# Kernel optimization log

Hardware: AMD Instinct MI355X
Metric: run time of the kernel (lower is better)

Reference implementation:

```python
import jax, jax.numpy as jnp
import numpy as np

DIM = 2048
NUM_HEADS = 16
NUM_KV_HEADS = 4
HEAD_DIM = DIM // NUM_HEADS  # 128
KV_DIM = NUM_KV_HEADS * HEAD_DIM  # 512
ROPE_BASE = 10000.0
RMS_EPS = float(np.finfo(np.float32).eps)  # torch F.rms_norm default eps


def _rotary_tables(seq_len, dtype):
    inv_freq = 1.0 / (ROPE_BASE ** (jnp.arange(0, HEAD_DIM, 2, dtype=jnp.float32) / HEAD_DIM))
    freqs = jnp.arange(seq_len, dtype=jnp.float32)[:, None] * inv_freq[None, :]  # [S, hd/2]
    return jnp.cos(freqs).astype(dtype), jnp.sin(freqs).astype(dtype)


def _apply_rotary(x, cos, sin):
    # x: [B, H, S, hd]; cos/sin: [S, hd/2] broadcast over B,H
    half = x.shape[-1] // 2
    x1, x2 = x[..., :half], x[..., half:]
    return jnp.concatenate((x1 * cos + x2 * sin, x2 * cos - x1 * sin), axis=-1)


def _rms_norm(x):
    var = jnp.mean(jnp.square(x), axis=-1, keepdims=True)
    return x * jax.lax.rsqrt(var + RMS_EPS)


def setup_inputs() -> dict:
    key = jax.random.key(0)
    k1, k2, k3 = jax.random.split(key, 3)
    B, S = 4, 2048
    x = jax.random.normal(k1, (B, S, DIM), dtype=jnp.float32)
    W_qkv = jax.random.normal(k2, (DIM, DIM + 2 * KV_DIM), dtype=jnp.float32) * (DIM ** -0.5)
    W_out = jax.random.normal(k3, (DIM, DIM), dtype=jnp.float32) * (DIM ** -0.5)
    return {"x": x, "W_qkv": W_qkv, "W_out": W_out}


def reference(x, W_qkv, W_out):
    B, S, _ = x.shape
    G = NUM_HEADS // NUM_KV_HEADS  # GQA group size
    qkv = x @ W_qkv  # [B, S, dim + 2*kv_dim]
    q = qkv[..., :DIM].reshape(B, S, NUM_HEADS, HEAD_DIM).transpose(0, 2, 1, 3)
    k = qkv[..., DIM:DIM + KV_DIM].reshape(B, S, NUM_KV_HEADS, HEAD_DIM).transpose(0, 2, 1, 3)
    v = qkv[..., DIM + KV_DIM:].reshape(B, S, NUM_KV_HEADS, HEAD_DIM).transpose(0, 2, 1, 3)
    q = _rms_norm(q)
    k = _rms_norm(k)
    cos, sin = _rotary_tables(S, q.dtype)
    q = _apply_rotary(q, cos, sin)
    k = _apply_rotary(k, cos, sin)
    # Grouped-query attention without repeating K/V
    qg = q.reshape(B, NUM_KV_HEADS, G, S, HEAD_DIM)
    scale = HEAD_DIM ** -0.5
    scores = jnp.einsum('bkgsd,bktd->bkgst', qg, k) * scale  # [B, Hkv, G, S, S]
    causal = jnp.tril(jnp.ones((S, S), dtype=bool))
    scores = jnp.where(causal, scores, jnp.finfo(scores.dtype).min)
    probs = jax.nn.softmax(scores, axis=-1)
    y = jnp.einsum('bkgst,bktd->bkgsd', probs, v)  # [B, Hkv, G, S, hd]
    y = y.reshape(B, NUM_HEADS, S, HEAD_DIM).transpose(0, 2, 1, 3).reshape(B, S, DIM)
    return y @ W_out
```

## Files before the change

### kernel.cpp

```cpp
#include <hip/hip_runtime.h>

#define DIM    2048
#define SEQ    2048
#define BATCH  4
#define NH     16
#define NKV    4
#define HD     128
#define QKVN   3072
#define ROWS   (BATCH*SEQ)

typedef __bf16 bf16;
typedef __bf16 bf16x2 __attribute__((ext_vector_type(2)));
typedef __bf16 bf16x4 __attribute__((ext_vector_type(4)));
typedef __bf16 bf16x8 __attribute__((ext_vector_type(8)));
typedef float  f32x4  __attribute__((ext_vector_type(4)));
typedef float  f32x16 __attribute__((ext_vector_type(16)));

typedef union { bf16x4 v; unsigned int u[2]; } b4u;
typedef union { bf16x8 v8; bf16x4 v4[2]; } b8u;

#define SL2E 0.12752365234813963f

__device__ __forceinline__ void gload_lds16(const void* g, void* l) {
  __builtin_amdgcn_global_load_lds(
      (const __attribute__((address_space(1))) void*)g,
      (__attribute__((address_space(3))) void*)l, 16, 0, 0);
}


__global__ void convert_f32_bf16(const float* __restrict__ in, bf16* __restrict__ out, int n) {
  int i = (blockIdx.x * 256 + threadIdx.x) * 4;
  if (i < n) {
    float4 v = *(const float4*)(in + i);
    bf16x4 t = {(bf16)v.x, (bf16)v.y, (bf16)v.z, (bf16)v.w};
    *(bf16x4*)(out + i) = t;
  }
}

__global__ void transpose_w(const float* __restrict__ in, bf16* __restrict__ out, int R, int C) {
  __shared__ float t[64][65];
  int c0 = blockIdx.x * 64, r0 = blockIdx.y * 64;
  int tx = threadIdx.x & 63, ty = threadIdx.x >> 6;
  for (int i = ty; i < 64; i += 4) t[i][tx] = in[(size_t)(r0 + i) * C + c0 + tx];
  __syncthreads();
  for (int i = ty; i < 64; i += 4) out[(size_t)(c0 + i) * R + r0 + tx] = (bf16)t[tx][i];
}

__global__ void transpose_v(const bf16* __restrict__ vb, bf16* __restrict__ vT) {
  __shared__ bf16 t[64][65];
  int z = blockIdx.z;
  const bf16* in = vb + (size_t)z * SEQ * HD;
  bf16* out = vT + (size_t)z * HD * SEQ;
  int d0 = blockIdx.x * 64, s0 = blockIdx.y * 64;
  int tx = threadIdx.x & 63, ty = threadIdx.x >> 6;
  for (int i = ty; i < 64; i += 4) t[i][tx] = in[(size_t)(s0 + i) * HD + d0 + tx];
  __syncthreads();
  for (int i = ty; i < 64; i += 4) out[(size_t)(d0 + i) * SEQ + s0 + tx] = t[tx][i];
}

__global__ void rope_tables(float* __restrict__ cosT, float* __restrict__ sinT) {
  int idx = blockIdx.x * 256 + threadIdx.x;
  int s = idx >> 6, j = idx & 63;
  float inv = powf(10000.0f, -(float)j * (1.0f / 64.0f));
  float ang = (float)s * inv;
  cosT[idx] = cosf(ang);
  sinT[idx] = sinf(ang);
}

template <typename OutT>
__global__ __launch_bounds__(256, 2) void gemm_bt(
    const bf16* __restrict__ A, const bf16* __restrict__ BT,
    OutT* __restrict__ C, int M, int N, int K) {
  __shared__ __align__(16) bf16 lA[128 * 32];
  __shared__ __align__(16) bf16 lB[128 * 32];
  const int tid = threadIdx.x;
  const int lane = tid & 63, wave = tid >> 6;
  const int quad = lane >> 4, l16 = lane & 15;
  const int tileM = blockIdx.y * 128, tileN = blockIdx.x * 128;
  const int wm = (wave >> 1) * 64, wn = (wave & 1) * 64;

  f32x4 acc[4][4] = {};

  for (int kt = 0; kt < K; kt += 32) {
    __syncthreads();
    {
      int g0 = tid, g1 = tid + 256;
      gload_lds16(A + (size_t)(tileM + (g0 >> 2)) * K + kt + (g0 & 3) * 8,
                  (char*)lA + wave * 1024);
      gload_lds16(A + (size_t)(tileM + (g1 >> 2)) * K + kt + (g1 & 3) * 8,
                  (char*)lA + 4096 + wave * 1024);
      gload_lds16(BT + (size_t)(tileN + (g0 >> 2)) * K + kt + (g0 & 3) * 8,
                  (char*)lB + wave * 1024);
      gload_lds16(BT + (size_t)(tileN + (g1 >> 2)) * K + kt + (g1 & 3) * 8,
                  (char*)lB + 4096 + wave * 1024);
    }
    __syncthreads();

    bf16x8 af[4], bfr[4];
#pragma unroll
    for (int i = 0; i < 4; ++i)
      af[i] = *(const bf16x8*)&lA[(wm + i * 16 + l16) * 32 + quad * 8];
#pragma unroll
    for (int j = 0; j < 4; ++j)
      bfr[j] = *(const bf16x8*)&lB[(wn + j * 16 + l16) * 32 + quad * 8];
#pragma unroll
    for (int i = 0; i < 4; ++i)
#pragma unroll
      for (int j = 0; j < 4; ++j)
        acc[i][j] = __builtin_amdgcn_mfma_f32_16x16x32_bf16(af[i], bfr[j], acc[i][j], 0, 0, 0);
  }

#pragma unroll
  for (int i = 0; i < 4; ++i)
#pragma unroll
    for (int j = 0; j < 4; ++j)
#pragma unroll
      for (int r = 0; r < 4; ++r) {
        int row = tileM + wm + i * 16 + quad * 4 + r;
        int col = tileN + wn + j * 16 + l16;
        C[(size_t)row * N + col] = (OutT)acc[i][j][r];
      }
}

__global__ __launch_bounds__(256) void rmsnorm_rope(
    const bf16* __restrict__ qkv, const float* __restrict__ cosT,
    const float* __restrict__ sinT, bf16* __restrict__ qb,
    bf16* __restrict__ kb, bf16* __restrict__ vb) {
  int wave = threadIdx.x >> 6, lane = threadIdx.x & 63;
  int task = blockIdx.x * 4 + wave;
  int row = task / 24, chunk = task % 24;
  int b = row >> 11, s = row & 2047;

  const bf16* src = qkv + (size_t)row * QKVN + chunk * 128 + lane * 2;
  bf16x2 v = *(const bf16x2*)src;
  bf16 o0, o1;
  if (chunk >= 20) {
    o0 = v[0]; o1 = v[1];
  } else {
    float x0 = (float)v[0], x1 = (float)v[1];
    float ss = x0 * x0 + x1 * x1;
#pragma unroll
    for (int off = 1; off < 64; off <<= 1) ss += __shfl_xor(ss, off);
    float rms = rsqrtf(ss * (1.0f / 128.0f) + 1.1920929e-07f);
    x0 *= rms; x1 *= rms;
    float p0 = __shfl_xor(x0, 32), p1 = __shfl_xor(x1, 32);
    int j0 = (lane & 31) * 2;
    float c0 = cosT[s * 64 + j0], c1 = cosT[s * 64 + j0 + 1];
    float s0 = sinT[s * 64 + j0], s1 = sinT[s * 64 + j0 + 1];
    float r0, r1;
    if (lane < 32) { r0 = x0 * c0 + p0 * s0; r1 = x1 * c1 + p1 * s1; }
    else           { r0 = x0 * c0 - p0 * s0; r1 = x1 * c1 - p1 * s1; }
    if (chunk < 16) { r0 *= SL2E; r1 *= SL2E; }
    o0 = (bf16)r0; o1 = (bf16)r1;
  }
  bf16* dst;
  int d = lane * 2;
  if (chunk < 16)      dst = qb + ((size_t)(b * NH + chunk) * SEQ + s) * HD + d;
  else if (chunk < 20) dst = kb + ((size_t)(b * NKV + (chunk - 16)) * SEQ + s) * HD + d;
  else                 dst = vb + ((size_t)(b * NKV + (chunk - 20)) * SEQ + s) * HD + d;
  bf16x2 t = {o0, o1};
  *(bf16x2*)dst = t;
}

__global__ __launch_bounds__(256, 2) void attn_kernel(
    const bf16* __restrict__ qb, const bf16* __restrict__ kb,
    const bf16* __restrict__ vTb, bf16* __restrict__ y) {
  __shared__ __align__(16) char sm[65536];
  bf16* lK = (bf16*)sm;
  bf16* lV = (bf16*)(sm + 32768);

  const int tid = threadIdx.x;
  const int lane = tid & 63, wave = tid >> 6;
  const int l32 = lane & 31, h = lane >> 5;
  const int pairI = blockIdx.x, hh = blockIdx.y, b = blockIdx.z;
  const int kvh = hh >> 2;

  const bf16* qh = qb + (size_t)(b * NH + hh) * SEQ * HD;
  const bf16* kh = kb + (size_t)(b * NKV + kvh) * SEQ * HD;
  const bf16* vh = vTb + (size_t)(b * NKV + kvh) * HD * SEQ;

  for (int t = 0; t < 2; ++t) {
    const int qt = t ? pairI : (15 - pairI);
    const int qtile = qt * 128;
    const int qrow = qtile + wave * 32 + l32;

    bf16x8 qf[8];
#pragma unroll
    for (int ks = 0; ks < 8; ++ks)
      qf[ks] = *(const bf16x8*)&qh[(size_t)qrow * HD + ks * 16 + h * 8];

    f32x16 oacc[4] = {};
    float psum = 0.f;

    for (int kv0 = 0; kv0 <= qtile; kv0 += 128) {
      __syncthreads();
#pragma unroll
      for (int inst = 0; inst < 8; ++inst) {
        int slot = inst * 256 + tid;
        int R = slot >> 4;
        int gg = (slot & 15) ^ (R & 15);
        gload_lds16(kh + (size_t)(kv0 + R) * HD + gg * 8, (char*)lK + inst * 4096 + wave * 1024);
        gload_lds16(vh + (size_t)R * SEQ + kv0 + gg * 8, (char*)lV + inst * 4096 + wave * 1024);
      }
      __syncthreads();

      const bool diag = (kv0 == qtile);
      const int kvbMax = diag ? (wave + 1) : 4;
      for (int kvb = 0; kvb < kvbMax; ++kvb) {
        f32x16 sacc = {};
#pragma unroll
        for (int ks = 0; ks < 8; ++ks) {
          int row = kvb * 32 + l32;
          const bf16x8 af = *(const bf16x8*)&lK[row * 128 + (((ks * 2 + h) ^ (row & 15)) << 3)];
          sacc = __builtin_amdgcn_mfma_f32_32x32x16_bf16(af, qf[ks], sacc, 0, 0, 0);
        }
        float p[16];
        const bool msk = diag && (kvb == wave);
#pragma unroll
        for (int r = 0; r < 16; ++r) {
          float v = sacc[r];
          if (msk) {
            int kv = kv0 + kvb * 32 + (r & 3) + 4 * h + 8 * (r >> 2);
            if (kv > qrow) v = -1e30f;
          }
          float e = exp2f(v);
          p[r] = e;
          psum += e;
        }
        b4u pk[4];
#pragma unroll
        for (int B = 0; B < 4; ++B) {
          bf16x4 t4 = {(bf16)p[4 * B], (bf16)p[4 * B + 1], (bf16)p[4 * B + 2], (bf16)p[4 * B + 3]};
          pk[B].v = t4;
        }
#pragma unroll
        for (int ss = 0; ss < 2; ++ss) {
          b4u own = pk[2 * ss + h];
          b4u send = pk[2 * ss + (h ^ 1)];
          b4u got;
          got.u[0] = __shfl_xor(send.u[0], 32);
          got.u[1] = __shfl_xor(send.u[1], 32);
          b8u fr;
          fr.v4[0] = h ? got.v : own.v;
          fr.v4[1] = h ? own.v : got.v;
          int ks2 = kvb * 2 + ss;
#pragma unroll
          for (int nd = 0; nd < 4; ++nd) {
            int row = nd * 32 + l32;
            const bf16x8 vf = *(const bf16x8*)&lV[row * 128 + (((ks2 * 2 + h) ^ (row & 15)) << 3)];
            oacc[nd] = __builtin_amdgcn_mfma_f32_32x32x16_bf16(fr.v8, vf, oacc[nd], 0, 0, 0);
          }
        }
      }
    }

    float lsum = psum + __shfl_xor(psum, 32);
#pragma unroll
    for (int r = 0; r < 16; ++r) {
      int ql = (r & 3) + 4 * h + 8 * (r >> 2);
      float li = 1.0f / __shfl(lsum, ql);
      size_t base = ((size_t)(b * SEQ + qtile + wave * 32 + ql)) * DIM + hh * HD;
#pragma unroll
      for (int nd = 0; nd < 4; ++nd)
        y[base + nd * 32 + l32] = (bf16)(oacc[nd][r] * li);
    }
  }
}


extern "C" void kernel_launch(void* const* d_in, const int* in_sizes, int n_in,
                              void* d_out, int out_size, void* d_ws, size_t ws_size,
                              hipStream_t stream) {
  const float* x    = (const float*)d_in[0];
  const float* Wqkv = (const float*)d_in[1];
  const float* Wout = (const float*)d_in[2];
  float* out = (float*)d_out;

  char* w = (char*)d_ws;
  auto carve = [&](size_t bytes) -> char* {
    char* p = w;
    w += (bytes + 255) & ~(size_t)255;
    return p;
  };
  bf16* xb   = (bf16*)carve((size_t)ROWS * DIM * 2);
  bf16* WqT  = (bf16*)carve((size_t)QKVN * DIM * 2);
  bf16* WoT  = (bf16*)carve((size_t)DIM * DIM * 2);
  bf16* qkv  = (bf16*)carve((size_t)ROWS * QKVN * 2);
  bf16* kbuf = (bf16*)carve((size_t)BATCH * NKV * SEQ * HD * 2);
  bf16* vbuf = (bf16*)carve((size_t)BATCH * NKV * SEQ * HD * 2);
  float* cosT = (float*)carve((size_t)SEQ * 64 * 4);
  float* sinT = (float*)carve((size_t)SEQ * 64 * 4);

  bf16* qbuf = xb;
  bf16* vT   = WqT;
  bf16* ybuf = qkv;

  convert_f32_bf16<<<ROWS * DIM / 1024, 256, 0, stream>>>(x, xb, ROWS * DIM);
  transpose_w<<<dim3(QKVN / 64, DIM / 64), 256, 0, stream>>>(Wqkv, WqT, DIM, QKVN);
  transpose_w<<<dim3(DIM / 64, DIM / 64), 256, 0, stream>>>(Wout, WoT, DIM, DIM);
  rope_tables<<<SEQ * 64 / 256, 256, 0, stream>>>(cosT, sinT);

  gemm_bt<bf16><<<dim3(QKVN / 128, ROWS / 128), 256, 0, stream>>>(xb, WqT, qkv, ROWS, QKVN, DIM);
  rmsnorm_rope<<<ROWS * 24 / 4, 256, 0, stream>>>(qkv, cosT, sinT, qbuf, kbuf, vbuf);
  transpose_v<<<dim3(HD / 64, SEQ / 64, BATCH * NKV), 256, 0, stream>>>(vbuf, vT);
  attn_kernel<<<dim3(8, NH, BATCH), 256, 0, stream>>>(qbuf, kbuf, vT, ybuf);
  gemm_bt<float><<<dim3(DIM / 128, ROWS / 128), 256, 0, stream>>>(ybuf, WoT, out, ROWS, DIM, DIM);
}
```

Before: 518.6 us.

## Halve attention KV tile and LDS, one query tile per block, higher occupancy

The attention kernel now stages 64-key K/V tiles instead of 128, halving shared memory to 32 KB and raising the launch-bounds occupancy hint from 2 to 4 blocks. Each block handles one 128-row query tile, with heavy tiles issued first, instead of a balanced pair of tiles, so the grid doubles. Causal skipping is now done per wave against each 32-key sub-block. This aims to hide memory and MFMA latency with more resident waves, at the cost of twice as many barrier-separated load phases and possibly less even per-block work.

New measurement: 783.4 us. 51.1% more time.

```diff
diff --git a/kernel.cpp b/kernel.cpp
--- a/kernel.cpp
+++ b/kernel.cpp
@@ -162,51 +162,58 @@
   *(bf16x2*)dst = t;
 }
 
-__global__ __launch_bounds__(256, 2) void attn_kernel(
+__global__ __launch_bounds__(256, 4) void attn_kernel(
     const bf16* __restrict__ qb, const bf16* __restrict__ kb,
     const bf16* __restrict__ vTb, bf16* __restrict__ y) {
-  __shared__ __align__(16) char sm[65536];
+  __shared__ __align__(16) char sm[32768];
   bf16* lK = (bf16*)sm;
-  bf16* lV = (bf16*)(sm + 32768);
+  bf16* lV = (bf16*)(sm + 16384);
 
   const int tid = threadIdx.x;
   const int lane = tid & 63, wave = tid >> 6;
   const int l32 = lane & 31, h = lane >> 5;
-  const int pairI = blockIdx.x, hh = blockIdx.y, b = blockIdx.z;
+  const int qt = 15 - (int)blockIdx.x;
+  const int hh = blockIdx.y, b = blockIdx.z;
   const int kvh = hh >> 2;
 
   const bf16* qh = qb + (size_t)(b * NH + hh) * SEQ * HD;
   const bf16* kh = kb + (size_t)(b * NKV + kvh) * SEQ * HD;
   const bf16* vh = vTb + (size_t)(b * NKV + kvh) * HD * SEQ;
 
-  for (int t = 0; t < 2; ++t) {
-    const int qt = t ? pairI : (15 - pairI);
-    const int qtile = qt * 128;
-    const int qrow = qtile + wave * 32 + l32;
-
-    bf16x8 qf[8];
-#pragma unroll
-    for (int ks = 0; ks < 8; ++ks)
-      qf[ks] = *(const bf16x8*)&qh[(size_t)qrow * HD + ks * 16 + h * 8];
-
-    f32x16 oacc[4] = {};
-    float psum = 0.f;
-
-    for (int kv0 = 0; kv0 <= qtile; kv0 += 128) {
-      __syncthreads();
-#pragma unroll
-      for (int inst = 0; inst < 8; ++inst) {
-        int slot = inst * 256 + tid;
-        int R = slot >> 4;
-        int gg = (slot & 15) ^ (R & 15);
-        gload_lds16(kh + (size_t)(kv0 + R) * HD + gg * 8, (char*)lK + inst * 4096 + wave * 1024);
-        gload_lds16(vh + (size_t)R * SEQ + kv0 + gg * 8, (char*)lV + inst * 4096 + wave * 1024);
-      }
-      __syncthreads();
-
-      const bool diag = (kv0 == qtile);
-      const int kvbMax = diag ? (wave + 1) : 4;
-      for (int kvb = 0; kvb < kvbMax; ++kvb) {
+  const int qtile = qt * 128;
+  const int rS = qtile + wave * 32;
+  const int qrow = rS + l32;
+
+  bf16x8 qf[8];
+#pragma unroll
+  for (int ks = 0; ks < 8; ++ks)
+    qf[ks] = *(const bf16x8*)&qh[(size_t)qrow * HD + ks * 16 + h * 8];
+
+  f32x16 oacc[4] = {};
+  float psum = 0.f;
+
+  for (int kv0 = 0; kv0 <= qtile + 64; kv0 += 64) {
+    __syncthreads();
+#pragma unroll
+    for (int inst = 0; inst < 4; ++inst) {
+      int slot = inst * 256 + tid;
+      int R = slot >> 4;
+      int gg = (slot & 15) ^ (R & 15);
+      gload_lds16(kh + (size_t)(kv0 + R) * HD + gg * 8, (char*)lK + inst * 4096 + wave * 1024);
+    }
+#pragma unroll
+    for (int inst = 0; inst < 4; ++inst) {
+      int slot = inst * 256 + tid;
+      int R = slot >> 3;
+      int gg = (slot & 7) ^ (R & 7);
+      gload_lds16(vh + (size_t)R * SEQ + kv0 + gg * 8, (char*)lV + inst * 4096 + wave * 1024);
+    }
+    __syncthreads();
+
+#pragma unroll
+    for (int kvb = 0; kvb < 2; ++kvb) {
+      const int kvS = kv0 + kvb * 32;
+      if (kvS <= rS) {
         f32x16 sacc = {};
 #pragma unroll
         for (int ks = 0; ks < 8; ++ks) {
@@ -215,12 +222,12 @@
           sacc = __builtin_amdgcn_mfma_f32_32x32x16_bf16(af, qf[ks], sacc, 0, 0, 0);
         }
         float p[16];
-        const bool msk = diag && (kvb == wave);
+        const bool msk = (kvS == rS);
 #pragma unroll
         for (int r = 0; r < 16; ++r) {
           float v = sacc[r];
           if (msk) {
-            int kv = kv0 + kvb * 32 + (r & 3) + 4 * h + 8 * (r >> 2);
+            int kv = kvS + (r & 3) + 4 * h + 8 * (r >> 2);
             if (kv > qrow) v = -1e30f;
           }
           float e = exp2f(v);
@@ -243,27 +250,27 @@
           b8u fr;
           fr.v4[0] = h ? got.v : own.v;
           fr.v4[1] = h ? own.v : got.v;
-          int ks2 = kvb * 2 + ss;
+          int gi = kvb * 4 + ss * 2 + h;
 #pragma unroll
           for (int nd = 0; nd < 4; ++nd) {
             int row = nd * 32 + l32;
-            const bf16x8 vf = *(const bf16x8*)&lV[row * 128 + (((ks2 * 2 + h) ^ (row & 15)) << 3)];
+            const bf16x8 vf = *(const bf16x8*)&lV[row * 64 + ((gi ^ (row & 7)) << 3)];
             oacc[nd] = __builtin_amdgcn_mfma_f32_32x32x16_bf16(fr.v8, vf, oacc[nd], 0, 0, 0);
           }
         }
       }
     }
-
-    float lsum = psum + __shfl_xor(psum, 32);
-#pragma unroll
-    for (int r = 0; r < 16; ++r) {
-      int ql = (r & 3) + 4 * h + 8 * (r >> 2);
-      float li = 1.0f / __shfl(lsum, ql);
-      size_t base = ((size_t)(b * SEQ + qtile + wave * 32 + ql)) * DIM + hh * HD;
-#pragma unroll
-      for (int nd = 0; nd < 4; ++nd)
-        y[base + nd * 32 + l32] = (bf16)(oacc[nd][r] * li);
-    }
+  }
+
+  float lsum = psum + __shfl_xor(psum, 32);
+#pragma unroll
+  for (int r = 0; r < 16; ++r) {
+    int ql = (r & 3) + 4 * h + 8 * (r >> 2);
+    float li = 1.0f / __shfl(lsum, ql);
+    size_t base = ((size_t)(b * SEQ + qtile + wave * 32 + ql)) * DIM + hh * HD;
+#pragma unroll
+    for (int nd = 0; nd < 4; ++nd)
+      y[base + nd * 32 + l32] = (bf16)(oacc[nd][r] * li);
   }
 }
 
@@ -303,6 +310,6 @@
   gemm_bt<bf16><<<dim3(QKVN / 128, ROWS / 128), 256, 0, stream>>>(xb, WqT, qkv, ROWS, QKVN, DIM);
   rmsnorm_rope<<<ROWS * 24 / 4, 256, 0, stream>>>(qkv, cosT, sinT, qbuf, kbuf, vbuf);
   transpose_v<<<dim3(HD / 64, SEQ / 64, BATCH * NKV), 256, 0, stream>>>(vbuf, vT);
-  attn_kernel<<<dim3(8, NH, BATCH), 256, 0, stream>>>(qbuf, kbuf, vT, ybuf);
+  attn_kernel<<<dim3(16, NH, BATCH), 256, 0, stream>>>(qbuf, kbuf, vT, ybuf);
   gemm_bt<float><<<dim3(DIM / 128, ROWS / 128), 256, 0, stream>>>(ybuf, WoT, out, ROWS, DIM, DIM);
 }
```
